# Kernel optimization log

Hardware: AMD Instinct MI355X
Metric: run time of the kernel (lower is better)

Reference implementation:

```python
import jax, jax.numpy as jnp
import numpy as np

N = 50000      # query points
M = 50000      # support points
H = 32         # max neighbors
K = 15         # kernel points
CIN = 64
COUT = 128
KP_EXTENT = 0.06
RADIUS = 0.05


def setup_inputs() -> dict:
    key = jax.random.key(0)
    k1, k2, k3, k4, k5, k6, k7 = jax.random.split(key, 7)
    # point coordinates in a small cube so neighbors fall within KP_extent of kernel points
    q_pts = jax.random.uniform(k1, (N, 3), dtype=jnp.float32) * 0.1
    s_pts = jax.random.uniform(k2, (M, 3), dtype=jnp.float32) * 0.1
    # indices in [0, M]; index M selects the shadow (padded) support point
    neighb_inds = jax.random.randint(k3, (N, H), 0, M + 1)
    x = jax.random.normal(k4, (M, CIN), dtype=jnp.float32)
    # kaiming-uniform-like init for [K, Cin, Cout] weights
    weights = jax.random.normal(k5, (K, CIN, COUT), dtype=jnp.float32) / np.sqrt(CIN)
    # kernel points uniformly in a sphere of radius RADIUS, center point fixed at origin
    d = jax.random.normal(k6, (K, 3), dtype=jnp.float32)
    d = d / jnp.linalg.norm(d, axis=1, keepdims=True)
    r = jax.random.uniform(k7, (K, 1), dtype=jnp.float32) ** (1.0 / 3.0) * RADIUS
    kernel_points = (d * r).at[0].set(0.0)
    return {"q_pts": q_pts, "s_pts": s_pts, "x": x, "weights": weights,
            "kernel_points": kernel_points, "neighb_inds": neighb_inds}


def reference(q_pts, s_pts, x, weights, kernel_points, neighb_inds):
    # pad support points with a far-away shadow point (matches torch: +1e6)
    s_pad = jnp.concatenate([s_pts, jnp.full((1, s_pts.shape[1]), 1e6, s_pts.dtype)], axis=0)
    # gather neighbor coords and center on queries: [N, H, 3]
    neighbors = s_pad[neighb_inds] - q_pts[:, None, :]
    # squared distances to each kernel point: [N, H, K]
    diff = neighbors[:, :, None, :] - kernel_points[None, None, :, :]
    sq_d = jnp.sum(diff * diff, axis=3)
    # linear influence, transposed to [N, K, H]
    h = jnp.maximum(1.0 - jnp.sqrt(sq_d) / KP_EXTENT, 0.0)
    h = jnp.swapaxes(h, 1, 2)
    # pad features with a zero row for shadow neighbors, then gather: [N, H, Cin]
    x_pad = jnp.concatenate([x, jnp.zeros((1, x.shape[1]), x.dtype)], axis=0)
    neighb_x = x_pad[neighb_inds]
    # project features onto kernel points: [N, K, Cin]
    fpk = jnp.einsum('nkh,nhc->nkc', h, neighb_x)
    # per-kernel-point matmul + sum over kernel points: [N, Cout]
    out = jnp.einsum('nkc,kco->no', fpk, weights)
    return out
```

## Files before the change

kernel.cpp:

```cpp
#include <hip/hip_runtime.h>

#define NQ     50000
#define MS     50000
#define NH     32
#define NK     15
#define CIN    64
#define COUT   128
#define QT     32
#define INV_EXT (1.0f/0.06f)

typedef unsigned int   uint32;
typedef unsigned short u16;
typedef _Float16 f16;
typedef _Float16 f16x8 __attribute__((ext_vector_type(8)));
typedef float    f32x4 __attribute__((ext_vector_type(4)));

#define WB_BYTES  (8*32*64*8*2)
#define XPH_BYTES (MS*CIN*2)

#if __has_builtin(__builtin_amdgcn_sqrtf)
#define SQRTF __builtin_amdgcn_sqrtf
#else
#define SQRTF sqrtf
#endif

__device__ __forceinline__ uint32 permlo(uint32 A, uint32 B) {
#if __has_builtin(__builtin_amdgcn_perm)
    return __builtin_amdgcn_perm(A, B, 0x01000504u);
#else
    return (A & 0xffffu) | (B << 16);
#endif
}
__device__ __forceinline__ uint32 permhi(uint32 A, uint32 B) {
#if __has_builtin(__builtin_amdgcn_perm)
    return __builtin_amdgcn_perm(A, B, 0x03020706u);
#else
    return (A >> 16) | (B & 0xffff0000u);
#endif
}

__device__ __forceinline__ u16 f16bits(float f) {
    return __builtin_bit_cast(u16, (f16)f);
}

__device__ __forceinline__ uint32 pk2(float a, float b) {
#if __has_builtin(__builtin_amdgcn_cvt_pkrtz)
    return __builtin_bit_cast(uint32, __builtin_amdgcn_cvt_pkrtz(a, b));
#else
    return (uint32)f16bits(a) | ((uint32)f16bits(b) << 16);
#endif
}


__global__ __launch_bounds__(256)
void pack_all(const float* __restrict__ x, u16* __restrict__ xph,
              const float* __restrict__ w, u16* __restrict__ wb) {
    const int bid = blockIdx.x;
    if (bid < 3125) {
        const int tid = bid * 256 + threadIdx.x;
        const int row = tid >> 4;
        const int lp  = tid & 15;
        const float v0 = x[row*CIN +  0 + lp];
        const float v1 = x[row*CIN + 16 + lp];
        const float v2 = x[row*CIN + 32 + lp];
        const float v3 = x[row*CIN + 48 + lp];
        uint2 d;
        d.x = pk2(v0, v1);
        d.y = pk2(v2, v3);
        *(uint2*)&xph[row*CIN + lp*4] = d;
    } else {
        const int u  = (bid - 3125) * 4 + (threadIdx.x >> 6);
        const int nt = u >> 5;
        const int ks = u & 31;
        const int l  = threadIdx.x & 63;
        u16 frag[8];
        #pragma unroll
        for (int e = 0; e < 8; ++e) {
            const int Kp = ks*32 + (l >> 4)*8 + e;
            const int c  = Kp >> 4;
            const int k  = Kp & 15;
            const float val = (k < NK) ? w[(k*CIN + c)*COUT + nt*16 + (l & 15)] : 0.0f;
            frag[e] = f16bits(val);
        }
        *(f16x8*)&wb[((nt*32 + ks)*64 + l)*8] = *(f16x8*)frag;
    }
}

__global__ __launch_bounds__(512, 4)
void kpconv_fused(const float* __restrict__ q_pts,
                  const float* __restrict__ s_pts,
                  const u16*  __restrict__ xph,
                  const u16*  __restrict__ wb,
                  const float* __restrict__ kp,
                  const int*   __restrict__ nind,
                  float* __restrict__ out)
{
    __shared__ u16   fpkAT[QT*1024];
    __shared__ float nb[QT*100];
    __shared__ u16   inds[QT*NH];

    const int t  = threadIdx.x;
    const int q0 = blockIdx.x * QT;

    #pragma unroll
    for (int p = t; p < QT*NH; p += 512) {
        const int q = p >> 5, j = p & 31;
        const int qg = q0 + q;
        const int qc = (qg < NQ) ? qg : (NQ - 1);
        const int ind = nind[qc*NH + j];
        const bool valid = (ind < MS);
        inds[p] = (u16)(valid ? ind : 0);
        float sx, sy, sz;
        if (valid) { sx = s_pts[ind*3+0]; sy = s_pts[ind*3+1]; sz = s_pts[ind*3+2]; }
        else       { sx = 1e6f; sy = 1e6f; sz = 1e6f; }
        nb[q*100 + j*3 + 0] = sx - q_pts[qc*3+0];
        nb[q*100 + j*3 + 1] = sy - q_pts[qc*3+1];
        nb[q*100 + j*3 + 2] = sz - q_pts[qc*3+2];
    }
    __syncthreads();

    {
        const int l  = t & 63, wv = t >> 6;
        const int lc = l & 15, lg = l >> 4;
        const int kc = (lc < NK) ? lc : (NK - 1);
        const float kx = kp[kc*3+0], ky = kp[kc*3+1], kz = kp[kc*3+2];
        const uint32 lcxor = (uint32)(lc & 4) << 2;

        uint2 v[4][8];
        #pragma unroll
        for (int qi = 0; qi < 4; ++qi) {
            const int q = wv*4 + qi;
            const uint4 iv = *(const uint4*)&inds[q*NH + lg*8];
            uint32 r[8];
            r[0] = iv.x & 0xffffu; r[1] = iv.x >> 16;
            r[2] = iv.y & 0xffffu; r[3] = iv.y >> 16;
            r[4] = iv.z & 0xffffu; r[5] = iv.z >> 16;
            r[6] = iv.w & 0xffffu; r[7] = iv.w >> 16;
            #pragma unroll
            for (int e = 0; e < 8; ++e)
                v[qi][e] = *(const uint2*)(xph + r[e]*CIN + lc*4);
        }

        #pragma unroll
        for (int qi = 0; qi < 4; ++qi) {
            const int q = wv*4 + qi;
            const float* nbq = &nb[q*100 + lg*24];
            const float4 r0 = *(const float4*)(nbq +  0);
            const float4 r1 = *(const float4*)(nbq +  4);
            const float4 r2 = *(const float4*)(nbq +  8);
            const float4 r3 = *(const float4*)(nbq + 12);
            const float4 r4 = *(const float4*)(nbq + 16);
            const float4 r5 = *(const float4*)(nbq + 20);
            float jx[8], jy[8], jz[8];
            jx[0]=r0.x; jy[0]=r0.y; jz[0]=r0.z;
            jx[1]=r0.w; jy[1]=r1.x; jz[1]=r1.y;
            jx[2]=r1.z; jy[2]=r1.w; jz[2]=r2.x;
            jx[3]=r2.y; jy[3]=r2.z; jz[3]=r2.w;
            jx[4]=r3.x; jy[4]=r3.y; jz[4]=r3.z;
            jx[5]=r3.w; jy[5]=r4.x; jz[5]=r4.y;
            jx[6]=r4.z; jy[6]=r4.w; jz[6]=r5.x;
            jx[7]=r5.y; jy[7]=r5.z; jz[7]=r5.w;
            float hh[8];
            #pragma unroll
            for (int e = 0; e < 8; ++e) {
                const float dx = jx[e] - kx;
                const float dy = jy[e] - ky;
                const float dz = jz[e] - kz;
                float h = 1.0f - SQRTF(dx*dx + dy*dy + dz*dz) * INV_EXT;
                hh[e] = (h > 0.0f) ? h : 0.0f;
            }
            uint32 ab[4];
            ab[0] = pk2(hh[0], hh[1]); ab[1] = pk2(hh[2], hh[3]);
            ab[2] = pk2(hh[4], hh[5]); ab[3] = pk2(hh[6], hh[7]);
            const f16x8 a = __builtin_bit_cast(f16x8, *(uint4*)ab);
            f32x4 acc0 = {0,0,0,0}, acc1 = {0,0,0,0}, acc2 = {0,0,0,0}, acc3 = {0,0,0,0};
            #pragma unroll
            for (int ct = 0; ct < 4; ++ct) {
                const uint32 A0 = (ct & 2) ? v[qi][0].y : v[qi][0].x, B0 = (ct & 2) ? v[qi][1].y : v[qi][1].x;
                const uint32 A1 = (ct & 2) ? v[qi][2].y : v[qi][2].x, B1 = (ct & 2) ? v[qi][3].y : v[qi][3].x;
                const uint32 A2 = (ct & 2) ? v[qi][4].y : v[qi][4].x, B2 = (ct & 2) ? v[qi][5].y : v[qi][5].x;
                const uint32 A3 = (ct & 2) ? v[qi][6].y : v[qi][6].x, B3 = (ct & 2) ? v[qi][7].y : v[qi][7].x;
                uint4 bd;
                if (ct & 1) {
                    bd.x = permhi(A0, B0); bd.y = permhi(A1, B1);
                    bd.z = permhi(A2, B2); bd.w = permhi(A3, B3);
                } else {
                    bd.x = permlo(A0, B0); bd.y = permlo(A1, B1);
                    bd.z = permlo(A2, B2); bd.w = permlo(A3, B3);
                }
                const f16x8 b = __builtin_bit_cast(f16x8, bd);
                if      (ct == 0) acc0 = __builtin_amdgcn_mfma_f32_16x16x32_f16(a, b, acc0, 0,0,0);
                else if (ct == 1) acc1 = __builtin_amdgcn_mfma_f32_16x16x32_f16(a, b, acc1, 0,0,0);
                else if (ct == 2) acc2 = __builtin_amdgcn_mfma_f32_16x16x32_f16(a, b, acc2, 0,0,0);
                else              acc3 = __builtin_amdgcn_mfma_f32_16x16x32_f16(a, b, acc3, 0,0,0);
            }
            {
                const uint32 wbase = ((uint32)(q*2048 + lc*32 + lg*8))
                                     ^ (((uint32)(q & 7)) << 4) ^ lcxor;
                char* wp = (char*)fpkAT + wbase;
                #pragma unroll
                for (int ct = 0; ct < 4; ++ct) {
                    const f32x4 av = (ct==0)?acc0:(ct==1)?acc1:(ct==2)?acc2:acc3;
                    uint2 dv;
                    dv.x = pk2(av[0], av[1]);
                    dv.y = pk2(av[2], av[3]);
                    *(uint2*)(wp + ct*512) = dv;
                }
            }
        }
    }

    const int l   = t & 63;
    const int nt  = t >> 6;
    const u16* bp = wb + (nt*32)*512 + l*8;
    uint4 pb0 = *(const uint4*)(bp + 0*512);
    uint4 pb1 = *(const uint4*)(bp + 1*512);
    uint4 pb2 = *(const uint4*)(bp + 2*512);
    uint4 pb3 = *(const uint4*)(bp + 3*512);

    __syncthreads();

    {
        const int col = l & 15;
        const int kg  = l >> 4;
        f32x4 acc0 = {0.f,0.f,0.f,0.f};
        f32x4 acc1 = {0.f,0.f,0.f,0.f};
        const uint32 b0 = ((uint32)(col*2048 + kg*16)) ^ (((uint32)(col & 7)) << 4);
        const char* base = (const char*)fpkAT;
        const char* p0 = base + (b0);
        const char* p1 = base + (b0 ^ 64u);
        const char* p2 = base + (b0 ^ 144u);
        const char* p3 = base + (b0 ^ 208u);
        #pragma unroll
        for (int ks = 0; ks < 32; ++ks) {
            const char* sel = ((ks & 3) == 0) ? p0 : ((ks & 3) == 1) ? p1
                            : ((ks & 3) == 2) ? p2 : p3;
            const int off = (ks >> 2) * 256;
            const f16x8 a0 = *(const f16x8*)(sel + off);
            const f16x8 a1 = *(const f16x8*)(sel + off + 32768);
            uint4 bd;
            if      (ks == 0) bd = pb0;
            else if (ks == 1) bd = pb1;
            else if (ks == 2) bd = pb2;
            else if (ks == 3) bd = pb3;
            else              bd = *(const uint4*)(bp + ks*512);
            const f16x8 b = __builtin_bit_cast(f16x8, bd);
            acc0 = __builtin_amdgcn_mfma_f32_16x16x32_f16(a0, b, acc0, 0, 0, 0);
            acc1 = __builtin_amdgcn_mfma_f32_16x16x32_f16(a1, b, acc1, 0, 0, 0);
        }
        const int rbase = kg * 4;
        #pragma unroll
        for (int r = 0; r < 4; ++r) {
            const int row0 = q0 + rbase + r;
            const int row1 = row0 + 16;
            if (row0 < NQ) out[row0*COUT + nt*16 + col] = acc0[r];
            if (row1 < NQ) out[row1*COUT + nt*16 + col] = acc1[r];
        }
    }
}

extern "C" void kernel_launch(void* const* d_in, const int* in_sizes, int n_in,
                              void* d_out, int out_size, void* d_ws, size_t ws_size,
                              hipStream_t stream) {
    const float* q_pts = (const float*)d_in[0];
    const float* s_pts = (const float*)d_in[1];
    const float* x     = (const float*)d_in[2];
    const float* wts   = (const float*)d_in[3];
    const float* kp    = (const float*)d_in[4];
    const int*   nind  = (const int*)d_in[5];
    float* out = (float*)d_out;

    u16* wbp = (u16*)d_ws;
    u16* xph = (u16*)((char*)d_ws + WB_BYTES);

    hipLaunchKernelGGL(pack_all, dim3(3125 + 64), dim3(256), 0, stream, x, xph, wts, wbp);
    hipLaunchKernelGGL(kpconv_fused, dim3((NQ + QT - 1) / QT), dim3(512), 0, stream,
                       q_pts, s_pts, xph, wbp, kp, nind, out);
}
```

Measured before the change: 60.81 us.

## Process two query tiles per block with overlapped projection and matmul phases

Each block now handles two 32-query tiles. The projection of the second tile is computed in registers while the first tile's weight matmul runs, then written to shared memory after a barrier. Neighbor offsets are stored in shared memory as fp16 and no longer as fp32, and neighbor indices are reread from global memory instead of being staged in shared memory. The aim is to hide gather latency behind the MFMA phase and cut shared memory use. In exchange the kernel runs half as many blocks, has more barriers and holds more live registers, and the fp16 offsets lose precision in the distance computation.

Result: slower. 78.29 us (+28.7%).

```diff
diff --git a/kernel.cpp b/kernel.cpp
--- a/kernel.cpp
+++ b/kernel.cpp
@@ -86,6 +86,8 @@
     }
 }
 
+struct BRes { uint2 d[8]; };
+
 __global__ __launch_bounds__(512, 4)
 void kpconv_fused(const float* __restrict__ q_pts,
                   const float* __restrict__ s_pts,
@@ -95,77 +97,65 @@
                   const int*   __restrict__ nind,
                   float* __restrict__ out)
 {
-    __shared__ u16   fpkAT[QT*1024];
-    __shared__ float nb[QT*100];
-    __shared__ u16   inds[QT*NH];
-
-    const int t  = threadIdx.x;
-    const int q0 = blockIdx.x * QT;
-
-    #pragma unroll
-    for (int p = t; p < QT*NH; p += 512) {
-        const int q = p >> 5, j = p & 31;
-        const int qg = q0 + q;
-        const int qc = (qg < NQ) ? qg : (NQ - 1);
-        const int ind = nind[qc*NH + j];
-        const bool valid = (ind < MS);
-        inds[p] = (u16)(valid ? ind : 0);
-        float sx, sy, sz;
-        if (valid) { sx = s_pts[ind*3+0]; sy = s_pts[ind*3+1]; sz = s_pts[ind*3+2]; }
-        else       { sx = 1e6f; sy = 1e6f; sz = 1e6f; }
-        nb[q*100 + j*3 + 0] = sx - q_pts[qc*3+0];
-        nb[q*100 + j*3 + 1] = sy - q_pts[qc*3+1];
-        nb[q*100 + j*3 + 2] = sz - q_pts[qc*3+2];
-    }
-    __syncthreads();
-
-    {
-        const int l  = t & 63, wv = t >> 6;
-        const int lc = l & 15, lg = l >> 4;
-        const int kc = (lc < NK) ? lc : (NK - 1);
-        const float kx = kp[kc*3+0], ky = kp[kc*3+1], kz = kp[kc*3+2];
-        const uint32 lcxor = (uint32)(lc & 4) << 2;
-
-        uint2 v[4][8];
-        #pragma unroll
-        for (int qi = 0; qi < 4; ++qi) {
-            const int q = wv*4 + qi;
-            const uint4 iv = *(const uint4*)&inds[q*NH + lg*8];
-            uint32 r[8];
-            r[0] = iv.x & 0xffffu; r[1] = iv.x >> 16;
-            r[2] = iv.y & 0xffffu; r[3] = iv.y >> 16;
-            r[4] = iv.z & 0xffffu; r[5] = iv.z >> 16;
-            r[6] = iv.w & 0xffffu; r[7] = iv.w >> 16;
-            #pragma unroll
-            for (int e = 0; e < 8; ++e)
-                v[qi][e] = *(const uint2*)(xph + r[e]*CIN + lc*4);
-        }
-
-        #pragma unroll
-        for (int qi = 0; qi < 4; ++qi) {
-            const int q = wv*4 + qi;
-            const float* nbq = &nb[q*100 + lg*24];
-            const float4 r0 = *(const float4*)(nbq +  0);
-            const float4 r1 = *(const float4*)(nbq +  4);
-            const float4 r2 = *(const float4*)(nbq +  8);
-            const float4 r3 = *(const float4*)(nbq + 12);
-            const float4 r4 = *(const float4*)(nbq + 16);
-            const float4 r5 = *(const float4*)(nbq + 20);
-            float jx[8], jy[8], jz[8];
-            jx[0]=r0.x; jy[0]=r0.y; jz[0]=r0.z;
-            jx[1]=r0.w; jy[1]=r1.x; jz[1]=r1.y;
-            jx[2]=r1.z; jy[2]=r1.w; jz[2]=r2.x;
-            jx[3]=r2.y; jy[3]=r2.z; jz[3]=r2.w;
-            jx[4]=r3.x; jy[4]=r3.y; jz[4]=r3.z;
-            jx[5]=r3.w; jy[5]=r4.x; jz[5]=r4.y;
-            jx[6]=r4.z; jy[6]=r4.w; jz[6]=r5.x;
-            jx[7]=r5.y; jy[7]=r5.z; jz[7]=r5.w;
+    __shared__ u16 fpkAT[QT*1024];
+    __shared__ u16 nbh[2][QT*96];
+
+    const int t   = threadIdx.x;
+    const int q00 = blockIdx.x * (2*QT);
+    const int q01 = q00 + QT;
+
+    const int l  = t & 63, wv = t >> 6;
+    const int lc = l & 15, lg = l >> 4;
+    const int kc = (lc < NK) ? lc : (NK - 1);
+    const float kx = kp[kc*3+0], ky = kp[kc*3+1], kz = kp[kc*3+2];
+    const uint32 lcxor = (uint32)(lc & 4) << 2;
+
+    auto STAGE = [&](int tl, int qb) {
+        #pragma unroll
+        for (int p = t; p < QT*NH; p += 512) {
+            const int q = p >> 5, j = p & 31;
+            const int qg = qb + q;
+            const int qc = (qg < NQ) ? qg : (NQ - 1);
+            const int ind = nind[qc*NH + j];
+            const bool valid = (ind < MS);
+            float sx, sy, sz;
+            if (valid) { sx = s_pts[ind*3+0]; sy = s_pts[ind*3+1]; sz = s_pts[ind*3+2]; }
+            else       { sx = 1e6f; sy = 1e6f; sz = 1e6f; }
+            u16* nq = &nbh[tl][q*96];
+            nq[0*32 + j] = f16bits(sx - q_pts[qc*3+0]);
+            nq[1*32 + j] = f16bits(sy - q_pts[qc*3+1]);
+            nq[2*32 + j] = f16bits(sz - q_pts[qc*3+2]);
+        }
+    };
+
+    auto B_PAIR = [&](int tl, int qb, int qloc) -> BRes {
+        BRes res;
+        #pragma unroll
+        for (int s = 0; s < 2; ++s) {
+            const int q  = qloc + s;
+            const int qg = qb + q;
+            const int qc = (qg < NQ) ? qg : (NQ - 1);
+            const int4 i0 = *(const int4*)(nind + qc*NH + lg*8);
+            const int4 i1 = *(const int4*)(nind + qc*NH + lg*8 + 4);
+            uint2 v[8];
+            {
+                const int rr[8] = { i0.x, i0.y, i0.z, i0.w, i1.x, i1.y, i1.z, i1.w };
+                #pragma unroll
+                for (int e = 0; e < 8; ++e) {
+                    const int ic = (rr[e] < MS) ? rr[e] : 0;
+                    v[e] = *(const uint2*)(xph + ic*CIN + lc*4);
+                }
+            }
+            const u16* nq = &nbh[tl][q*96];
+            const f16x8 xs = *(const f16x8*)&nq[0*32 + lg*8];
+            const f16x8 ys = *(const f16x8*)&nq[1*32 + lg*8];
+            const f16x8 zs = *(const f16x8*)&nq[2*32 + lg*8];
             float hh[8];
             #pragma unroll
             for (int e = 0; e < 8; ++e) {
-                const float dx = jx[e] - kx;
-                const float dy = jy[e] - ky;
-                const float dz = jz[e] - kz;
+                const float dx = (float)xs[e] - kx;
+                const float dy = (float)ys[e] - ky;
+                const float dz = (float)zs[e] - kz;
                 float h = 1.0f - SQRTF(dx*dx + dy*dy + dz*dz) * INV_EXT;
                 hh[e] = (h > 0.0f) ? h : 0.0f;
             }
@@ -176,10 +166,10 @@
             f32x4 acc0 = {0,0,0,0}, acc1 = {0,0,0,0}, acc2 = {0,0,0,0}, acc3 = {0,0,0,0};
             #pragma unroll
             for (int ct = 0; ct < 4; ++ct) {
-                const uint32 A0 = (ct & 2) ? v[qi][0].y : v[qi][0].x, B0 = (ct & 2) ? v[qi][1].y : v[qi][1].x;
-                const uint32 A1 = (ct & 2) ? v[qi][2].y : v[qi][2].x, B1 = (ct & 2) ? v[qi][3].y : v[qi][3].x;
-                const uint32 A2 = (ct & 2) ? v[qi][4].y : v[qi][4].x, B2 = (ct & 2) ? v[qi][5].y : v[qi][5].x;
-                const uint32 A3 = (ct & 2) ? v[qi][6].y : v[qi][6].x, B3 = (ct & 2) ? v[qi][7].y : v[qi][7].x;
+                const uint32 A0 = (ct & 2) ? v[0].y : v[0].x, B0 = (ct & 2) ? v[1].y : v[1].x;
+                const uint32 A1 = (ct & 2) ? v[2].y : v[2].x, B1 = (ct & 2) ? v[3].y : v[3].x;
+                const uint32 A2 = (ct & 2) ? v[4].y : v[4].x, B2 = (ct & 2) ? v[5].y : v[5].x;
+                const uint32 A3 = (ct & 2) ? v[6].y : v[6].x, B3 = (ct & 2) ? v[7].y : v[7].x;
                 uint4 bd;
                 if (ct & 1) {
                     bd.x = permhi(A0, B0); bd.y = permhi(A1, B1);
@@ -194,38 +184,37 @@
                 else if (ct == 2) acc2 = __builtin_amdgcn_mfma_f32_16x16x32_f16(a, b, acc2, 0,0,0);
                 else              acc3 = __builtin_amdgcn_mfma_f32_16x16x32_f16(a, b, acc3, 0,0,0);
             }
-            {
-                const uint32 wbase = ((uint32)(q*2048 + lc*32 + lg*8))
-                                     ^ (((uint32)(q & 7)) << 4) ^ lcxor;
-                char* wp = (char*)fpkAT + wbase;
-                #pragma unroll
-                for (int ct = 0; ct < 4; ++ct) {
-                    const f32x4 av = (ct==0)?acc0:(ct==1)?acc1:(ct==2)?acc2:acc3;
-                    uint2 dv;
-                    dv.x = pk2(av[0], av[1]);
-                    dv.y = pk2(av[2], av[3]);
-                    *(uint2*)(wp + ct*512) = dv;
-                }
-            }
-        }
-    }
-
-    const int l   = t & 63;
-    const int nt  = t >> 6;
-    const u16* bp = wb + (nt*32)*512 + l*8;
-    uint4 pb0 = *(const uint4*)(bp + 0*512);
-    uint4 pb1 = *(const uint4*)(bp + 1*512);
-    uint4 pb2 = *(const uint4*)(bp + 2*512);
-    uint4 pb3 = *(const uint4*)(bp + 3*512);
-
-    __syncthreads();
-
-    {
-        const int col = l & 15;
-        const int kg  = l >> 4;
+            #pragma unroll
+            for (int ct = 0; ct < 4; ++ct) {
+                const f32x4 av = (ct==0)?acc0:(ct==1)?acc1:(ct==2)?acc2:acc3;
+                uint2 dv;
+                dv.x = pk2(av[0], av[1]);
+                dv.y = pk2(av[2], av[3]);
+                res.d[s*4 + ct] = dv;
+            }
+        }
+        return res;
+    };
+
+    auto B_WRITE = [&](int qloc, const BRes& res) {
+        #pragma unroll
+        for (int s = 0; s < 2; ++s) {
+            const int q = qloc + s;
+            const uint32 wbase = ((uint32)(q*2048 + lc*32 + lg*8))
+                                 ^ (((uint32)(q & 7)) << 4) ^ lcxor;
+            char* wp = (char*)fpkAT + wbase;
+            #pragma unroll
+            for (int ct = 0; ct < 4; ++ct)
+                *(uint2*)(wp + ct*512) = res.d[s*4 + ct];
+        }
+    };
+
+    auto CPHASE = [&](int qb) {
+        const int nt = wv;
+        const u16* bp = wb + (nt*32)*512 + l*8;
         f32x4 acc0 = {0.f,0.f,0.f,0.f};
         f32x4 acc1 = {0.f,0.f,0.f,0.f};
-        const uint32 b0 = ((uint32)(col*2048 + kg*16)) ^ (((uint32)(col & 7)) << 4);
+        const uint32 b0 = ((uint32)(lc*2048 + lg*16)) ^ (((uint32)(lc & 7)) << 4);
         const char* base = (const char*)fpkAT;
         const char* p0 = base + (b0);
         const char* p1 = base + (b0 ^ 64u);
@@ -238,25 +227,43 @@
             const int off = (ks >> 2) * 256;
             const f16x8 a0 = *(const f16x8*)(sel + off);
             const f16x8 a1 = *(const f16x8*)(sel + off + 32768);
-            uint4 bd;
-            if      (ks == 0) bd = pb0;
-            else if (ks == 1) bd = pb1;
-            else if (ks == 2) bd = pb2;
-            else if (ks == 3) bd = pb3;
-            else              bd = *(const uint4*)(bp + ks*512);
+            const uint4 bd = *(const uint4*)(bp + ks*512);
             const f16x8 b = __builtin_bit_cast(f16x8, bd);
             acc0 = __builtin_amdgcn_mfma_f32_16x16x32_f16(a0, b, acc0, 0, 0, 0);
             acc1 = __builtin_amdgcn_mfma_f32_16x16x32_f16(a1, b, acc1, 0, 0, 0);
         }
-        const int rbase = kg * 4;
+        const int rbase = lg * 4;
         #pragma unroll
         for (int r = 0; r < 4; ++r) {
-            const int row0 = q0 + rbase + r;
+            const int row0 = qb + rbase + r;
             const int row1 = row0 + 16;
-            if (row0 < NQ) out[row0*COUT + nt*16 + col] = acc0[r];
-            if (row1 < NQ) out[row1*COUT + nt*16 + col] = acc1[r];
-        }
+            if (row0 < NQ) out[row0*COUT + nt*16 + lc] = acc0[r];
+            if (row1 < NQ) out[row1*COUT + nt*16 + lc] = acc1[r];
+        }
+    };
+
+    STAGE(0, q00);
+    __syncthreads();
+
+    {
+        const BRes r0 = B_PAIR(0, q00, wv*4 + 0);
+        B_WRITE(wv*4 + 0, r0);
+        const BRes r1 = B_PAIR(0, q00, wv*4 + 2);
+        B_WRITE(wv*4 + 2, r1);
+        STAGE(1, q01);
     }
+    __syncthreads();
+
+    CPHASE(q00);
+    const BRes h0 = B_PAIR(1, q01, wv*4 + 0);
+    const BRes h1 = B_PAIR(1, q01, wv*4 + 2);
+    __syncthreads();
+
+    B_WRITE(wv*4 + 0, h0);
+    B_WRITE(wv*4 + 2, h1);
+    __syncthreads();
+
+    CPHASE(q01);
 }
 
 extern "C" void kernel_launch(void* const* d_in, const int* in_sizes, int n_in,
@@ -274,6 +281,6 @@
     u16* xph = (u16*)((char*)d_ws + WB_BYTES);
 
     hipLaunchKernelGGL(pack_all, dim3(3125 + 64), dim3(256), 0, stream, x, xph, wts, wbp);
-    hipLaunchKernelGGL(kpconv_fused, dim3((NQ + QT - 1) / QT), dim3(512), 0, stream,
+    hipLaunchKernelGGL(kpconv_fused, dim3((NQ + 2*QT - 1) / (2*QT)), dim3(512), 0, stream,
                        q_pts, s_pts, xph, wbp, kp, nind, out);
 }
```
